# Optimization experiments

Hardware: AMD Instinct MI355X
Metric: run time of the kernel (lower is better)

Reference implementation:

```python
import jax, jax.numpy as jnp
import numpy as np

N, C, H, W = 8, 80, 200, 200
PRE_NMS_THRESH = 0.05
PRE_NMS_TOP_N = 1000
NMS_THRESH = 0.6
FPN_POST_NMS_TOP_N = 100
MIN_SIZE = 0.0
TO_REMOVE = 1.0
CLASS_OFFSET = 100000.0  # > any coordinate; separates classes for class-aware NMS


def setup_inputs() -> dict:
    key = jax.random.key(0)
    k1, k2, k3, k4, k5 = jax.random.split(key, 5)
    # logits shifted so sigmoid probs sit near the 0.05 threshold (realistic sparsity)
    box_cls = jax.random.normal(k1, (N, C, H, W), jnp.float32) - 3.0
    box_regression = jax.random.uniform(k2, (N, 4, H, W), jnp.float32) * 64.0
    centerness = jax.random.normal(k3, (N, 1, H, W), jnp.float32)
    locations = jax.random.uniform(k4, (H * W, 2), jnp.float32) * 1600.0
    image_sizes = jax.random.randint(k5, (N, 2), 800, 1600, jnp.int32)  # (h, w)
    return {"locations": locations, "box_cls": box_cls,
            "box_regression": box_regression, "centerness": centerness,
            "image_sizes": image_sizes}


def _pairwise_iou(boxes):
    x1, y1, x2, y2 = boxes[:, 0], boxes[:, 1], boxes[:, 2], boxes[:, 3]
    area = (x2 - x1 + TO_REMOVE) * (y2 - y1 + TO_REMOVE)  # [K]
    iw = jnp.clip(jnp.minimum(x2[:, None], x2[None, :]) - jnp.maximum(x1[:, None], x1[None, :]) + TO_REMOVE, 0.0)
    ih = jnp.clip(jnp.minimum(y2[:, None], y2[None, :]) - jnp.maximum(y1[:, None], y1[None, :]) + TO_REMOVE, 0.0)
    inter = iw * ih
    return inter / (area[:, None] + area[None, :] - inter)


def reference(locations, box_cls, box_regression, centerness, image_sizes):
    n, c, h, w = box_cls.shape
    # [N,C,H,W] -> [N,HW,C] probs; [N,4,H,W] -> [N,HW,4]; centerness -> [N,HW]
    cls_prob = jax.nn.sigmoid(box_cls.transpose(0, 2, 3, 1).reshape(n, -1, c))
    reg = box_regression.transpose(0, 2, 3, 1).reshape(n, -1, 4)
    cent = jax.nn.sigmoid(centerness.transpose(0, 2, 3, 1).reshape(n, -1))

    def per_image(p, r, ct, hw):
        # candidate mask on raw class probs (before centerness weighting), as in source
        cand = p > PRE_NMS_THRESH                      # [HW, C]
        scores = p * ct[:, None]                       # [HW, C]
        flat = jnp.where(cand, scores, -jnp.inf).reshape(-1)
        top_s, top_i = jax.lax.top_k(flat, PRE_NMS_TOP_N)   # sorted desc
        loc_idx = top_i // c
        labels = top_i % c + 1
        valid = top_s > 0.0
        l2 = locations[loc_idx]                        # [K, 2]
        rr = r[loc_idx]                                # [K, 4]
        boxes = jnp.concatenate([l2 - rr[:, :2], l2 + rr[:, 2:]], axis=-1)
        ih = hw[0].astype(jnp.float32)
        iw = hw[1].astype(jnp.float32)
        boxes = jnp.stack([jnp.clip(boxes[:, 0], 0.0, iw - 1.0),
                           jnp.clip(boxes[:, 1], 0.0, ih - 1.0),
                           jnp.clip(boxes[:, 2], 0.0, iw - 1.0),
                           jnp.clip(boxes[:, 3], 0.0, ih - 1.0)], axis=-1)
        bw = boxes[:, 2] - boxes[:, 0] + TO_REMOVE
        bh = boxes[:, 3] - boxes[:, 1] + TO_REMOVE
        valid = valid & (bw >= MIN_SIZE) & (bh >= MIN_SIZE)
        # class-aware NMS via per-class coordinate offset
        ob = boxes + labels.astype(jnp.float32)[:, None] * CLASS_OFFSET
        iou = _pairwise_iou(ob)                        # [K, K]
        K = PRE_NMS_TOP_N
        idxs = jnp.arange(K)
        def body(supp, i):
            keep_i = valid[i] & jnp.logical_not(supp[i])
            supp = supp | (keep_i & (iou[i] > NMS_THRESH) & (idxs != i))
            return supp, keep_i
        _, keep = jax.lax.scan(body, jnp.zeros(K, dtype=bool), idxs)
        fscores = jnp.where(keep & valid, top_s, -jnp.inf)
        fs, fi = jax.lax.top_k(fscores, FPN_POST_NMS_TOP_N)
        fv = fs > 0.0
        fb = boxes[fi] * fv[:, None].astype(boxes.dtype)
        fl = jnp.where(fv, labels[fi], 0).astype(jnp.float32)
        out_s = jnp.where(fv, jnp.sqrt(jnp.where(fv, fs, 1.0)), 0.0)  # sqrt of cls*centerness
        # [K_post, 6] = x1,y1,x2,y2,score,label
        return jnp.concatenate([fb, out_s[:, None], fl[:, None]], axis=-1)

    return jax.vmap(per_image)(cls_prob, reg, cent, image_sizes)
```

## Files before the change

### kernel.cpp

```cpp
#include <hip/hip_runtime.h>
#include <math.h>

#define NIMG 8
#define NCLS 80
#define HW 40000
#define M (NCLS*HW)
#define UBINS 4096
#define CANDL 4096
#define SPILL_CAP 65536
#define BCAP 1024
#define TOPK 1000
#define OUTK 100
#define PRE_T 0.05f
#define NMS_T 0.6f
#define FLOOR_BITS 0x3E800000u
#define FLOOR_SAFE 0.2494f

__device__ unsigned int       g_scnt[NIMG][32];
__device__ unsigned int       g_ovf[NIMG];
__device__ float              g_xthr[NIMG * HW];
__device__ float              g_sct[NIMG * HW];
__device__ unsigned long long g_key[NIMG][SPILL_CAP];

__device__ __forceinline__ float sigmoid_exact(float x){
    return 1.0f / (1.0f + expf(-x));
}

__device__ __forceinline__ unsigned long long shfl_xor_u64(unsigned long long v, int j){
    int lo = __shfl_xor((int)(unsigned int)(v & 0xffffffffull), j);
    int hi = __shfl_xor((int)(unsigned int)(v >> 32), j);
    return ((unsigned long long)(unsigned int)hi << 32) | (unsigned long long)(unsigned int)lo;
}

__global__ void k0_init(const float* __restrict__ cent){
    int t = blockIdx.x * blockDim.x + threadIdx.x;
    if (t < NIMG * 32) ((unsigned int*)g_scnt)[t] = 0u;
    if (t < NIMG) g_ovf[t] = 0u;
    if (t < NIMG * HW){
        float pct = sigmoid_exact(cent[t]);
        g_sct[t] = pct;
        float a = FLOOR_SAFE / pct;
        float xt;
        if (a >= 1.0f) xt = 3.0e38f;
        else {
            float am = fminf(a, 0.98f);
            xt = logf(am / (1.0f - am));
        }
        g_xthr[t] = xt;
    }
}

__global__ void __launch_bounds__(1024) k1_spill(const float* __restrict__ cls){
    const int n   = blockIdx.y;
    const int tid = threadIdx.x;
    const int e0  = blockIdx.x * 4096 + tid * 4;
    __shared__ unsigned long long skey[BCAP];
    __shared__ unsigned int lcnt, lbase;
    if (tid == 0) lcnt = 0u;
    __syncthreads();
    if (e0 < M){
        const int c  = e0 / HW;
        const int hw = e0 - c * HW;
        float4 x  = *(const float4*)(cls + (size_t)n * M + e0);
        float4 th = *(const float4*)(g_xthr + n * HW + hw);
        #define SPILL1(J, XV) \
        if (XV >= (J==0?th.x:J==1?th.y:J==2?th.z:th.w)){ \
            float p_ = sigmoid_exact(XV); \
            if (p_ > PRE_T){ \
                float s_ = p_ * g_sct[n * HW + hw + J]; \
                unsigned long long key_ = ((unsigned long long)__float_as_uint(s_) << 32) \
                    | (unsigned long long)(0xFFFFFFFFu - (unsigned int)((hw + J) * NCLS + c)); \
                unsigned int pp_ = atomicAdd(&lcnt, 1u); \
                if (pp_ < BCAP) skey[pp_] = key_; \
            } \
        }
        SPILL1(0, x.x)
        SPILL1(1, x.y)
        SPILL1(2, x.z)
        SPILL1(3, x.w)
        #undef SPILL1
    }
    __syncthreads();
    unsigned int raw = lcnt;
    unsigned int cnt = raw < BCAP ? raw : BCAP;
    if (tid == 0){
        lbase = cnt ? atomicAdd(&g_scnt[n][0], cnt) : 0u;
        if (raw > BCAP) g_ovf[n] = 1u;
    }
    __syncthreads();
    unsigned int base = lbase;
    for (unsigned int i = tid; i < cnt; i += 1024){
        unsigned int pos = base + i;
        if (pos < SPILL_CAP) g_key[n][pos] = skey[i];
    }
}

struct SelPhase {
    unsigned int hist[UBINS];
    unsigned int cs[256];
    unsigned int wtot[4];
    unsigned long long keysL[CANDL];
};
struct NmsPhase {
    float ox1[TOPK], oy1[TOPK], ox2[TOPK], oy2[TOPK], oar[TOPK];
    float bxs[TOPK][4];
    float sc[TOPK];
    int   lab[TOPK];
    int   keeplist[OUTK];
    unsigned int  Wc[16][80];
    unsigned int  ctot[80];
    unsigned int  coff[81];
    unsigned int  wcnt[16];
    unsigned short ord[1024];
    unsigned char validf[TOPK];
    unsigned char supp[TOPK];
    unsigned char keepf[1024];
};
union KU { SelPhase sel; NmsPhase nms; };

#define REGSTEP(K_, J_) { \
    unsigned long long pa = shfl_xor_u64(va, (J_)); \
    unsigned long long pb = shfl_xor_u64(vb, (J_)); \
    bool fa = ((tid & (J_)) == 0); \
    bool da = ((tid & (K_)) == 0); \
    bool db = (((tid + 1024) & (K_)) == 0); \
    va = (fa == da) ? (va > pa ? va : pa) : (va < pa ? va : pa); \
    vb = (fa == db) ? (vb > pb ? vb : pb) : (vb < pb ? vb : pb); \
}

__global__ void __launch_bounds__(1024) k2_select_nms(const float* __restrict__ cls,
                                                      const float* __restrict__ loc,
                                                      const float* __restrict__ reg,
                                                      const int*   __restrict__ imsz,
                                                      float* __restrict__ out){
    const int n = blockIdx.x;
    const int tid = threadIdx.x;
    const int lane = tid & 63;
    const int wv   = tid >> 6;
    __shared__ KU u;
    __shared__ unsigned long long stop[TOPK];
    __shared__ unsigned int lcnt, s_cut, s_flag, s_nmsfb, s_cnt, s_c, s_csn, s_Cest, s_srtbad;

    for (int i = tid; i < UBINS; i += 1024) u.sel.hist[i] = 0u;
    if (tid == 0){ s_nmsfb = 0u; s_srtbad = 0u; s_c = 0xFFFFFFFFu; s_csn = 0u;
                   s_Cest = 0u; s_cut = 0u; lcnt = 0u; }
    if (tid < TOPK) stop[tid] = 0ull;
    __syncthreads();

    unsigned int scnt_raw = g_scnt[n][0];
    unsigned int ovf_f    = g_ovf[n];
    unsigned int S = scnt_raw < SPILL_CAP ? scnt_raw : SPILL_CAP;

    for (unsigned int i = tid; i < S; i += 1024){
        unsigned long long k = g_key[n][i];
        float s = __uint_as_float((unsigned int)(k >> 32));
        atomicAdd(&u.sel.hist[(int)(s * 4096.0f)], 1u);
    }
    __syncthreads();
    if (tid < 256){
        unsigned int s = 0;
        int base = tid * 16;
        #pragma unroll
        for (int i = 0; i < 16; ++i) s += u.sel.hist[base + i];
        u.sel.cs[tid] = s;
    }
    __syncthreads();
    if (tid < 256){
        unsigned int v = u.sel.cs[tid];
        #pragma unroll
        for (int d = 1; d < 64; d <<= 1){
            unsigned int t = __shfl_down(v, d);
            if (lane + d < 64) v += t;
        }
        if (lane == 0) u.sel.wtot[wv] = v;
        u.sel.cs[tid] = v;
    }
    __syncthreads();
    if (tid < 256){
        unsigned int tail = 0;
        for (int w = wv + 1; w < 4; ++w) tail += u.sel.wtot[w];
        u.sel.cs[tid] += tail;
    }
    __syncthreads();
    if (tid < 256){
        unsigned int a = u.sel.cs[tid];
        unsigned int b = (tid == 255) ? 0u : u.sel.cs[tid + 1];
        if (a >= TOPK && b < TOPK){ s_c = (unsigned int)tid; s_csn = b; }
    }
    __syncthreads();
    if (wv == 0 && s_c != 0xFFFFFFFFu){
        unsigned int cst = s_c;
        unsigned int h = (lane < 16) ? u.sel.hist[cst * 16 + lane] : 0u;
        #pragma unroll
        for (int d = 1; d < 16; d <<= 1){
            unsigned int t = __shfl_down(h, d);
            if (lane + d < 16) h += t;
        }
        unsigned int gs  = h + s_csn;
        unsigned int gsn = __shfl_down(gs, 1);
        if (lane == 15) gsn = s_csn;
        if (lane < 16 && gs >= TOPK && gsn < TOPK){ s_cut = cst * 16 + lane; s_Cest = gs; }
    }
    __syncthreads();
    if (tid == 0){
        unsigned int c025 = u.sel.cs[64];
        s_flag = (scnt_raw > SPILL_CAP) || ovf_f || (s_c == 0xFFFFFFFFu) ||
                 (c025 < TOPK) || (s_Cest > CANDL) ? 1u : 0u;
    }
    __syncthreads();

    if (s_flag){
        for (int i = tid; i < UBINS; i += 1024) u.sel.hist[i] = 0u;
        __syncthreads();
        const float* cls_n = cls + (size_t)n * M;
        const float* sct_n = g_sct + n * HW;
        for (int e = tid; e < M; e += 1024){
            float p = sigmoid_exact(cls_n[e]);
            if (p > PRE_T){
                int c = e / HW; int hw = e - c * HW;
                float s = p * sct_n[hw];
                atomicAdd(&u.sel.hist[(int)(s * 4096.0f)], 1u);
            }
        }
        __syncthreads();
        if (tid < 256){
            unsigned int s = 0;
            int base = tid * 16;
            #pragma unroll
            for (int i = 0; i < 16; ++i) s += u.sel.hist[base + i];
            u.sel.cs[tid] = s;
        }
        __syncthreads();
        if (tid == 0){
            unsigned int acc = 0; int cut = 0; int c = 255;
            for (; c >= 0; --c){ if (acc + u.sel.cs[c] >= TOPK) break; acc += u.sel.cs[c]; }
            if (c >= 0){
                int b = c*16 + 15;
                for (;; --b){ acc += u.sel.hist[b]; if (acc >= TOPK || b == c*16) break; }
                cut = b;
            }
            while (acc > CANDL && cut < UBINS){ acc -= u.sel.hist[cut]; cut++; }
            s_cut = (unsigned int)cut;
        }
        __syncthreads();
        unsigned int cutb = s_cut;
        for (int e = tid; e < M; e += 1024){
            float p = sigmoid_exact(cls_n[e]);
            if (p > PRE_T){
                int c = e / HW; int hw = e - c * HW;
                float s = p * sct_n[hw];
                if ((int)(s * 4096.0f) >= (int)cutb){
                    unsigned int pos = atomicAdd(&lcnt, 1u);
                    if (pos < CANDL){
                        unsigned int idx = (unsigned int)(hw * NCLS + c);
                        u.sel.keysL[pos] = ((unsigned long long)__float_as_uint(s) << 32)
                                         | (unsigned long long)(0xFFFFFFFFu - idx);
                    }
                }
            }
        }
    } else {
        unsigned int cutb = s_cut;
        for (unsigned int i = tid; i < S; i += 1024){
            unsigned long long k = g_key[n][i];
            float s = __uint_as_float((unsigned int)(k >> 32));
            bool pass = ((unsigned int)(int)(s * 4096.0f)) >= cutb;
            unsigned long long mb = __ballot(pass);
            unsigned int wcnt_ = (unsigned int)__popcll(mb);
            unsigned int base = 0;
            if (lane == 0 && wcnt_) base = atomicAdd(&lcnt, wcnt_);
            base = (unsigned int)__builtin_amdgcn_readfirstlane((int)base);
            if (pass){
                unsigned int p = base + (unsigned int)__popcll(mb & ((1ull << lane) - 1ull));
                if (p < CANDL) u.sel.keysL[p] = k;
            }
        }
    }
    __syncthreads();

    int C = (int)(lcnt < CANDL ? lcnt : CANDL);
    unsigned long long kk = 0ull;
    if (C <= 2048){
        for (int i = C + tid; i < 2048; i += 1024) u.sel.keysL[i] = 0ull;
        __syncthreads();
        unsigned long long va = u.sel.keysL[tid];
        unsigned long long vb = u.sel.keysL[tid + 1024];
        REGSTEP(2,1)
        REGSTEP(4,2)  REGSTEP(4,1)
        REGSTEP(8,4)  REGSTEP(8,2)  REGSTEP(8,1)
        REGSTEP(16,8) REGSTEP(16,4) REGSTEP(16,2) REGSTEP(16,1)
        REGSTEP(32,16) REGSTEP(32,8) REGSTEP(32,4) REGSTEP(32,2) REGSTEP(32,1)
        REGSTEP(64,32) REGSTEP(64,16) REGSTEP(64,8) REGSTEP(64,4) REGSTEP(64,2) REGSTEP(64,1)
        for (int k = 128; k <= 2048; k <<= 1){
            if (k == 2048){
                unsigned long long mx = va > vb ? va : vb;
                unsigned long long mn = va > vb ? vb : va;
                va = mx; vb = mn;
            }
            u.sel.keysL[tid] = va; u.sel.keysL[tid + 1024] = vb;
            __syncthreads();
            for (int j = (k == 2048) ? 512 : (k >> 1); j >= 64; j >>= 1){
                int i  = ((tid & ~(j - 1)) << 1) | (tid & (j - 1));
                int p2 = i | j;
                unsigned long long a = u.sel.keysL[i];
                unsigned long long b = u.sel.keysL[p2];
                bool up = ((i & k) == 0);
                if (up ? (a < b) : (a > b)){ u.sel.keysL[i] = b; u.sel.keysL[p2] = a; }
                __syncthreads();
            }
            va = u.sel.keysL[tid]; vb = u.sel.keysL[tid + 1024];
            REGSTEP(k,32) REGSTEP(k,16) REGSTEP(k,8) REGSTEP(k,4) REGSTEP(k,2) REGSTEP(k,1)
        }
        u.sel.keysL[tid] = va; u.sel.keysL[tid + 1024] = vb;
        __syncthreads();
        bool bad = (u.sel.keysL[tid] < u.sel.keysL[tid + 1]);
        if (tid <= 1022) bad = bad || (u.sel.keysL[tid + 1024] < u.sel.keysL[tid + 1025]);
        if (bad) atomicOr(&s_srtbad, 1u);
        __syncthreads();
        if (s_srtbad){
            if (tid == 0) lcnt = 0u;
            __syncthreads();
            unsigned int cutb = s_cut;
            if (s_flag){
                const float* cls_n = cls + (size_t)n * M;
                const float* sct_n = g_sct + n * HW;
                for (int e = tid; e < M; e += 1024){
                    float p = sigmoid_exact(cls_n[e]);
                    if (p > PRE_T){
                        int c = e / HW; int hw = e - c * HW;
                        float s = p * sct_n[hw];
                        if ((int)(s * 4096.0f) >= (int)cutb){
                            unsigned int pos = atomicAdd(&lcnt, 1u);
                            if (pos < CANDL){
                                unsigned int idx = (unsigned int)(hw * NCLS + c);
                                u.sel.keysL[pos] = ((unsigned long long)__float_as_uint(s) << 32)
                                                 | (unsigned long long)(0xFFFFFFFFu - idx);
                            }
                        }
                    }
                }
            } else {
                for (unsigned int i = tid; i < S; i += 1024){
                    unsigned long long k = g_key[n][i];
                    float s = __uint_as_float((unsigned int)(k >> 32));
                    bool pass = ((unsigned int)(int)(s * 4096.0f)) >= cutb;
                    unsigned long long mb = __ballot(pass);
                    unsigned int wcnt_ = (unsigned int)__popcll(mb);
                    unsigned int base = 0;
                    if (lane == 0 && wcnt_) base = atomicAdd(&lcnt, wcnt_);
                    base = (unsigned int)__builtin_amdgcn_readfirstlane((int)base);
                    if (pass){
                        unsigned int p = base + (unsigned int)__popcll(mb & ((1ull << lane) - 1ull));
                        if (p < CANDL) u.sel.keysL[p] = k;
                    }
                }
            }
            __syncthreads();
            int C2 = (int)(lcnt < CANDL ? lcnt : CANDL);
            for (int i = C2 + tid; i < 2048; i += 1024) u.sel.keysL[i] = 0ull;
            __syncthreads();
            for (int k = 2; k <= 2048; k <<= 1){
                for (int j = k >> 1; j > 0; j >>= 1){
                    int i  = ((tid & ~(j - 1)) << 1) | (tid & (j - 1));
                    int p2 = i | j;
                    unsigned long long a = u.sel.keysL[i];
                    unsigned long long b = u.sel.keysL[p2];
                    bool up = ((i & k) == 0);
                    if (up ? (a < b) : (a > b)){ u.sel.keysL[i] = b; u.sel.keysL[p2] = a; }
                    __syncthreads();
                }
            }
        }
        kk = (tid < TOPK) ? u.sel.keysL[tid] : 0ull;
    } else {
        for (int i = tid; i < C; i += 1024){
            unsigned long long k = u.sel.keysL[i];
            int rank = 0;
            for (int j = 0; j < C; ++j) rank += (u.sel.keysL[j] > k) ? 1 : 0;
            if (rank < TOPK) stop[rank] = k;
        }
        __syncthreads();
        kk = (tid < TOPK) ? stop[tid] : 0ull;
    }
    __syncthreads();

    float rx1 = 0.f, ry1 = 0.f, rx2 = -1.f, ry2 = -1.f, rar = 1.f;
    float ihh = (float)imsz[2*n + 0];
    float iww = (float)imsz[2*n + 1];

    u.nms.keepf[tid] = 0;
    { unsigned int* wz = &u.nms.Wc[0][0];
      for (int i = tid; i < 16*80; i += 1024) wz[i] = 0u; }

    if (tid < TOPK){
        unsigned int bits = (unsigned int)(kk >> 32);
        float s = __uint_as_float(bits);
        u.nms.supp[tid] = 0;
        if (s > 0.0f){
            unsigned int idx = 0xFFFFFFFFu - (unsigned int)(kk & 0xFFFFFFFFull);
            int hw = (int)(idx / NCLS);
            int c  = (int)(idx % NCLS);
            int l  = c + 1;
            float x  = loc[2*hw], y = loc[2*hw + 1];
            float r0 = reg[((size_t)n*4 + 0)*HW + hw];
            float r1 = reg[((size_t)n*4 + 1)*HW + hw];
            float r2 = reg[((size_t)n*4 + 2)*HW + hw];
            float r3 = reg[((size_t)n*4 + 3)*HW + hw];
            float x1 = fminf(fmaxf(x - r0, 0.0f), iww - 1.0f);
            float y1 = fminf(fmaxf(y - r1, 0.0f), ihh - 1.0f);
            float x2 = fminf(fmaxf(x + r2, 0.0f), iww - 1.0f);
            float y2 = fminf(fmaxf(y + r3, 0.0f), ihh - 1.0f);
            u.nms.bxs[tid][0] = x1; u.nms.bxs[tid][1] = y1;
            u.nms.bxs[tid][2] = x2; u.nms.bxs[tid][3] = y2;
            float off = (float)l * 100000.0f;
            float a1 = x1 + off, b1 = y1 + off, a2 = x2 + off, b2 = y2 + off;
            float ar = (a2 - a1 + 1.0f) * (b2 - b1 + 1.0f);
            u.nms.ox1[tid] = a1; u.nms.oy1[tid] = b1;
            u.nms.ox2[tid] = a2; u.nms.oy2[tid] = b2; u.nms.oar[tid] = ar;
            rx1 = a1; ry1 = b1; rx2 = a2; ry2 = b2; rar = ar;
            u.nms.sc[tid] = s; u.nms.lab[tid] = l; u.nms.validf[tid] = 1;
        } else {
            u.nms.validf[tid] = 0; u.nms.sc[tid] = 0.0f; u.nms.lab[tid] = 0;
            u.nms.bxs[tid][0] = u.nms.bxs[tid][1] = 0.0f;
            u.nms.bxs[tid][2] = u.nms.bxs[tid][3] = 0.0f;
            u.nms.ox1[tid] = 0.f; u.nms.oy1[tid] = 0.f;
            u.nms.ox2[tid] = -1.f; u.nms.oy2[tid] = -1.f; u.nms.oar[tid] = 1.f;
        }
    }
    __syncthreads();

    int mk = -1;
    if (tid < TOPK && u.nms.validf[tid]) mk = u.nms.lab[tid] - 1;
    if (mk >= 0) atomicAdd(&u.nms.Wc[wv][mk], 1u);
    __syncthreads();
    if (tid < NCLS){
        unsigned int acc = 0;
        for (int w = 0; w < 16; ++w){
            unsigned int v = u.nms.Wc[w][tid];
            u.nms.Wc[w][tid] = acc;
            acc += v;
        }
        u.nms.ctot[tid] = acc;
        if (acc > 64) atomicOr(&s_nmsfb, 1u);
    }
    __syncthreads();
    if (wv == 0){
        unsigned int v = u.nms.ctot[lane];
        unsigned int inc = v;
        #pragma unroll
        for (int d = 1; d < 64; d <<= 1){
            unsigned int t = __shfl_up(inc, d);
            if (lane >= d) inc += t;
        }
        u.nms.coff[lane + 1] = inc;
        if (lane == 0) u.nms.coff[0] = 0u;
        unsigned int base = __shfl(inc, 63);
        unsigned int inc2 = (lane < 16) ? u.nms.ctot[64 + lane] : 0u;
        #pragma unroll
        for (int d = 1; d < 16; d <<= 1){
            unsigned int t = __shfl_up(inc2, d);
            if (lane >= d) inc2 += t;
        }
        if (lane < 16) u.nms.coff[65 + lane] = base + inc2;
    }
    __syncthreads();

    if (!s_nmsfb){
        int below = 0;
        for (int l = 0; l < 64; ++l){
            int ok = __shfl(mk, l);
            below += (l < lane && ok == mk) ? 1 : 0;
        }
        if (mk >= 0){
            unsigned int pos = u.nms.coff[mk] + u.nms.Wc[wv][mk] + (unsigned int)below;
            u.nms.ord[pos] = (unsigned short)tid;
        }
        __syncthreads();

        for (int k = wv; k < NCLS; k += 16){
            int base = (int)u.nms.coff[k];
            int ck   = (int)u.nms.coff[k + 1] - base;
            if (ck <= 0) continue;
            int rr = (lane < ck) ? (int)u.nms.ord[base + lane] : -1;
            float bx1 = 0.f, by1 = 0.f, bx2 = -1.f, by2 = -1.f, bar = 1.f;
            if (rr >= 0){
                bx1 = u.nms.ox1[rr]; by1 = u.nms.oy1[rr];
                bx2 = u.nms.ox2[rr]; by2 = u.nms.oy2[rr]; bar = u.nms.oar[rr];
            }
            int sup = 0;
            for (int p = 0; p < ck; ++p){
                int keep_p = !__shfl(sup, p);
                if (keep_p){
                    float px1 = __shfl(bx1, p), py1 = __shfl(by1, p);
                    float px2 = __shfl(bx2, p), py2 = __shfl(by2, p);
                    float par = __shfl(bar, p);
                    if (lane > p && rr >= 0){
                        float ix1 = fmaxf(px1, bx1);
                        float iy1 = fmaxf(py1, by1);
                        float ix2 = fminf(px2, bx2);
                        float iy2 = fminf(py2, by2);
                        float iw_ = fmaxf(ix2 - ix1 + 1.0f, 0.0f);
                        float ih_ = fmaxf(iy2 - iy1 + 1.0f, 0.0f);
                        float inter = iw_ * ih_;
                        float iou = inter / (par + bar - inter);
                        if (iou > NMS_T) sup = 1;
                    }
                }
            }
            if (rr >= 0) u.nms.keepf[rr] = sup ? 0 : 1;
        }
        __syncthreads();

        int kf = (int)u.nms.keepf[tid];
        unsigned long long mb = __ballot(kf != 0);
        if (lane == 0) u.nms.wcnt[wv] = (unsigned int)__popcll(mb);
        __syncthreads();
        if (wv == 0){
            unsigned int v = (lane < 16) ? u.nms.wcnt[lane] : 0u;
            unsigned int orig = v;
            for (int d = 1; d < 16; d <<= 1){
                unsigned int t = __shfl_up(v, d);
                if (lane >= d) v += t;
            }
            if (lane < 16) u.nms.wcnt[lane] = v - orig;
            if (lane == 15) s_cnt = (v < OUTK ? v : OUTK);
        }
        __syncthreads();
        if (kf){
            unsigned int slot = u.nms.wcnt[wv] + (unsigned int)__popcll(mb & ((1ull << lane) - 1ull));
            if (slot < OUTK) u.nms.keeplist[slot] = tid;
        }
    } else {
        int cnt = 0;
        for (int i = 0; i < TOPK; ++i){
            bool keep_i = u.nms.validf[i] && !u.nms.supp[i];
            if (keep_i){
                if (tid == 0) u.nms.keeplist[cnt] = i;
                if (tid < TOPK && tid != i){
                    float ix1 = fmaxf(u.nms.ox1[i], rx1);
                    float iy1 = fmaxf(u.nms.oy1[i], ry1);
                    float ix2 = fminf(u.nms.ox2[i], rx2);
                    float iy2 = fminf(u.nms.oy2[i], ry2);
                    float iw_ = fmaxf(ix2 - ix1 + 1.0f, 0.0f);
                    float ih_ = fmaxf(iy2 - iy1 + 1.0f, 0.0f);
                    float inter = iw_ * ih_;
                    float iou = inter / (u.nms.oar[i] + rar - inter);
                    if (iou > NMS_T) u.nms.supp[tid] = 1;
                }
                cnt++;
                __syncthreads();
                if (cnt == OUTK) break;
            }
        }
        if (tid == 0) s_cnt = (unsigned int)(cnt < OUTK ? cnt : OUTK);
    }
    __syncthreads();

    int cnt = (int)s_cnt;
    if (tid < OUTK){
        float r0=0.f,r1=0.f,r2=0.f,r3=0.f,r4=0.f,r5=0.f;
        if (tid < cnt){
            int i = u.nms.keeplist[tid];
            r0 = u.nms.bxs[i][0]; r1 = u.nms.bxs[i][1];
            r2 = u.nms.bxs[i][2]; r3 = u.nms.bxs[i][3];
            r4 = sqrtf(u.nms.sc[i]); r5 = (float)u.nms.lab[i];
        }
        float* o = out + ((size_t)n*OUTK + tid)*6;
        o[0]=r0; o[1]=r1; o[2]=r2; o[3]=r3; o[4]=r4; o[5]=r5;
    }
}

extern "C" void kernel_launch(void* const* d_in, const int* in_sizes, int n_in,
                              void* d_out, int out_size, void* d_ws, size_t ws_size,
                              hipStream_t stream){
    const float* loc  = (const float*)d_in[0];
    const float* cls  = (const float*)d_in[1];
    const float* reg  = (const float*)d_in[2];
    const float* cent = (const float*)d_in[3];
    const int*   imsz = (const int*)d_in[4];
    float* out = (float*)d_out;

    hipLaunchKernelGGL(k0_init,       dim3(625),                 dim3(512),  0, stream, cent);
    hipLaunchKernelGGL(k1_spill,      dim3((M+4095)/4096, NIMG), dim3(1024), 0, stream, cls);
    hipLaunchKernelGGL(k2_select_nms, dim3(NIMG),                dim3(1024), 0, stream,
                       cls, loc, reg, imsz, out);
}
```

Measured before the change: 257.0 us.

## Build score histogram in spill kernel and add 1024-wide register bitonic sort

```diff
diff --git a/kernel.cpp b/kernel.cpp
--- a/kernel.cpp
+++ b/kernel.cpp
@@ -18,6 +18,7 @@
 
 __device__ unsigned int       g_scnt[NIMG][32];
 __device__ unsigned int       g_ovf[NIMG];
+__device__ unsigned int       g_hist[NIMG][UBINS];
 __device__ float              g_xthr[NIMG * HW];
 __device__ float              g_sct[NIMG * HW];
 __device__ unsigned long long g_key[NIMG][SPILL_CAP];
@@ -36,6 +37,7 @@
     int t = blockIdx.x * blockDim.x + threadIdx.x;
     if (t < NIMG * 32) ((unsigned int*)g_scnt)[t] = 0u;
     if (t < NIMG) g_ovf[t] = 0u;
+    if (t < NIMG * UBINS) ((unsigned int*)g_hist)[t] = 0u;
     if (t < NIMG * HW){
         float pct = sigmoid_exact(cent[t]);
         g_sct[t] = pct;
@@ -70,6 +72,7 @@
                 float s_ = p_ * g_sct[n * HW + hw + J]; \
                 unsigned long long key_ = ((unsigned long long)__float_as_uint(s_) << 32) \
                     | (unsigned long long)(0xFFFFFFFFu - (unsigned int)((hw + J) * NCLS + c)); \
+                atomicAdd(&g_hist[n][(int)(s_ * 4096.0f)], 1u); \
                 unsigned int pp_ = atomicAdd(&lcnt, 1u); \
                 if (pp_ < BCAP) skey[pp_] = key_; \
             } \
@@ -127,6 +130,12 @@
     va = (fa == da) ? (va > pa ? va : pa) : (va < pa ? va : pa); \
     vb = (fa == db) ? (vb > pb ? vb : pb) : (vb < pb ? vb : pb); \
 }
+#define REGSTEP1(K_, J_) { \
+    unsigned long long pa = shfl_xor_u64(va, (J_)); \
+    bool fa = ((tid & (J_)) == 0); \
+    bool da = ((tid & (K_)) == 0); \
+    va = (fa == da) ? (va > pa ? va : pa) : (va < pa ? va : pa); \
+}
 
 __global__ void __launch_bounds__(1024) k2_select_nms(const float* __restrict__ cls,
                                                       const float* __restrict__ loc,
@@ -141,7 +150,7 @@
     __shared__ unsigned long long stop[TOPK];
     __shared__ unsigned int lcnt, s_cut, s_flag, s_nmsfb, s_cnt, s_c, s_csn, s_Cest, s_srtbad;
 
-    for (int i = tid; i < UBINS; i += 1024) u.sel.hist[i] = 0u;
+    for (int i = tid; i < UBINS; i += 1024) u.sel.hist[i] = g_hist[n][i];
     if (tid == 0){ s_nmsfb = 0u; s_srtbad = 0u; s_c = 0xFFFFFFFFu; s_csn = 0u;
                    s_Cest = 0u; s_cut = 0u; lcnt = 0u; }
     if (tid < TOPK) stop[tid] = 0ull;
@@ -151,12 +160,6 @@
     unsigned int ovf_f    = g_ovf[n];
     unsigned int S = scnt_raw < SPILL_CAP ? scnt_raw : SPILL_CAP;
 
-    for (unsigned int i = tid; i < S; i += 1024){
-        unsigned long long k = g_key[n][i];
-        float s = __uint_as_float((unsigned int)(k >> 32));
-        atomicAdd(&u.sel.hist[(int)(s * 4096.0f)], 1u);
-    }
-    __syncthreads();
     if (tid < 256){
         unsigned int s = 0;
         int base = tid * 16;
@@ -280,7 +283,38 @@
 
     int C = (int)(lcnt < CANDL ? lcnt : CANDL);
     unsigned long long kk = 0ull;
-    if (C <= 2048){
+    if (C <= 1024){
+        for (int i = C + tid; i < 1024; i += 1024) u.sel.keysL[i] = 0ull;
+        __syncthreads();
+        unsigned long long va = u.sel.keysL[tid];
+        REGSTEP1(2,1)
+        REGSTEP1(4,2)  REGSTEP1(4,1)
+        REGSTEP1(8,4)  REGSTEP1(8,2)  REGSTEP1(8,1)
+        REGSTEP1(16,8) REGSTEP1(16,4) REGSTEP1(16,2) REGSTEP1(16,1)
+        REGSTEP1(32,16) REGSTEP1(32,8) REGSTEP1(32,4) REGSTEP1(32,2) REGSTEP1(32,1)
+        REGSTEP1(64,32) REGSTEP1(64,16) REGSTEP1(64,8) REGSTEP1(64,4) REGSTEP1(64,2) REGSTEP1(64,1)
+        for (int k = 128; k <= 1024; k <<= 1){
+            u.sel.keysL[tid] = va;
+            __syncthreads();
+            for (int j = k >> 1; j >= 64; j >>= 1){
+                if (tid < 512){
+                    int i  = ((tid & ~(j - 1)) << 1) | (tid & (j - 1));
+                    int p2 = i | j;
+                    unsigned long long a = u.sel.keysL[i];
+                    unsigned long long b = u.sel.keysL[p2];
+                    bool up = ((i & k) == 0);
+                    if (up ? (a < b) : (a > b)){ u.sel.keysL[i] = b; u.sel.keysL[p2] = a; }
+                }
+                __syncthreads();
+            }
+            va = u.sel.keysL[tid];
+            REGSTEP1(k,32) REGSTEP1(k,16) REGSTEP1(k,8) REGSTEP1(k,4) REGSTEP1(k,2) REGSTEP1(k,1)
+        }
+        u.sel.keysL[tid] = va;
+        __syncthreads();
+        if (tid <= 1022 && u.sel.keysL[tid] < u.sel.keysL[tid + 1]) atomicOr(&s_srtbad, 1u);
+        __syncthreads();
+    } else if (C <= 2048){
         for (int i = C + tid; i < 2048; i += 1024) u.sel.keysL[i] = 0ull;
         __syncthreads();
         unsigned long long va = u.sel.keysL[tid];
@@ -317,61 +351,6 @@
         if (tid <= 1022) bad = bad || (u.sel.keysL[tid + 1024] < u.sel.keysL[tid + 1025]);
         if (bad) atomicOr(&s_srtbad, 1u);
         __syncthreads();
-        if (s_srtbad){
-            if (tid == 0) lcnt = 0u;
-            __syncthreads();
-            unsigned int cutb = s_cut;
-            if (s_flag){
-                const float* cls_n = cls + (size_t)n * M;
-                const float* sct_n = g_sct + n * HW;
-                for (int e = tid; e < M; e += 1024){
-                    float p = sigmoid_exact(cls_n[e]);
-                    if (p > PRE_T){
-                        int c = e / HW; int hw = e - c * HW;
-                        float s = p * sct_n[hw];
-                        if ((int)(s * 4096.0f) >= (int)cutb){
-                            unsigned int pos = atomicAdd(&lcnt, 1u);
-                            if (pos < CANDL){
-                                unsigned int idx = (unsigned int)(hw * NCLS + c);
-                                u.sel.keysL[pos] = ((unsigned long long)__float_as_uint(s) << 32)
-                                                 | (unsigned long long)(0xFFFFFFFFu - idx);
-                            }
-                        }
-                    }
-                }
-            } else {
-                for (unsigned int i = tid; i < S; i += 1024){
-                    unsigned long long k = g_key[n][i];
-                    float s = __uint_as_float((unsigned int)(k >> 32));
-                    bool pass = ((unsigned int)(int)(s * 4096.0f)) >= cutb;
-                    unsigned long long mb = __ballot(pass);
-                    unsigned int wcnt_ = (unsigned int)__popcll(mb);
-                    unsigned int base = 0;
-                    if (lane == 0 && wcnt_) base = atomicAdd(&lcnt, wcnt_);
-                    base = (unsigned int)__builtin_amdgcn_readfirstlane((int)base);
-                    if (pass){
-                        unsigned int p = base + (unsigned int)__popcll(mb & ((1ull << lane) - 1ull));
-                        if (p < CANDL) u.sel.keysL[p] = k;
-                    }
-                }
-            }
-            __syncthreads();
-            int C2 = (int)(lcnt < CANDL ? lcnt : CANDL);
-            for (int i = C2 + tid; i < 2048; i += 1024) u.sel.keysL[i] = 0ull;
-            __syncthreads();
-            for (int k = 2; k <= 2048; k <<= 1){
-                for (int j = k >> 1; j > 0; j >>= 1){
-                    int i  = ((tid & ~(j - 1)) << 1) | (tid & (j - 1));
-                    int p2 = i | j;
-                    unsigned long long a = u.sel.keysL[i];
-                    unsigned long long b = u.sel.keysL[p2];
-                    bool up = ((i & k) == 0);
-                    if (up ? (a < b) : (a > b)){ u.sel.keysL[i] = b; u.sel.keysL[p2] = a; }
-                    __syncthreads();
-                }
-            }
-        }
-        kk = (tid < TOPK) ? u.sel.keysL[tid] : 0ull;
     } else {
         for (int i = tid; i < C; i += 1024){
             unsigned long long k = u.sel.keysL[i];
@@ -380,8 +359,65 @@
             if (rank < TOPK) stop[rank] = k;
         }
         __syncthreads();
-        kk = (tid < TOPK) ? stop[tid] : 0ull;
-    }
+        if (tid < TOPK) u.sel.keysL[tid] = stop[tid];
+        __syncthreads();
+    }
+
+    if (s_srtbad){
+        if (tid == 0) lcnt = 0u;
+        __syncthreads();
+        unsigned int cutb = s_cut;
+        if (s_flag){
+            const float* cls_n = cls + (size_t)n * M;
+            const float* sct_n = g_sct + n * HW;
+            for (int e = tid; e < M; e += 1024){
+                float p = sigmoid_exact(cls_n[e]);
+                if (p > PRE_T){
+                    int c = e / HW; int hw = e - c * HW;
+                    float s = p * sct_n[hw];
+                    if ((int)(s * 4096.0f) >= (int)cutb){
+                        unsigned int pos = atomicAdd(&lcnt, 1u);
+                        if (pos < CANDL){
+                            unsigned int idx = (unsigned int)(hw * NCLS + c);
+                            u.sel.keysL[pos] = ((unsigned long long)__float_as_uint(s) << 32)
+                                             | (unsigned long long)(0xFFFFFFFFu - idx);
+                        }
+                    }
+                }
+            }
+        } else {
+            for (unsigned int i = tid; i < S; i += 1024){
+                unsigned long long k = g_key[n][i];
+                float s = __uint_as_float((unsigned int)(k >> 32));
+                bool pass = ((unsigned int)(int)(s * 4096.0f)) >= cutb;
+                unsigned long long mb = __ballot(pass);
+                unsigned int wcnt_ = (unsigned int)__popcll(mb);
+                unsigned int base = 0;
+                if (lane == 0 && wcnt_) base = atomicAdd(&lcnt, wcnt_);
+                base = (unsigned int)__builtin_amdgcn_readfirstlane((int)base);
+                if (pass){
+                    unsigned int p = base + (unsigned int)__popcll(mb & ((1ull << lane) - 1ull));
+                    if (p < CANDL) u.sel.keysL[p] = k;
+                }
+            }
+        }
+        __syncthreads();
+        int C2 = (int)(lcnt < CANDL ? lcnt : CANDL);
+        for (int i = C2 + tid; i < 2048; i += 1024) u.sel.keysL[i] = 0ull;
+        __syncthreads();
+        for (int k = 2; k <= 2048; k <<= 1){
+            for (int j = k >> 1; j > 0; j >>= 1){
+                int i  = ((tid & ~(j - 1)) << 1) | (tid & (j - 1));
+                int p2 = i | j;
+                unsigned long long a = u.sel.keysL[i];
+                unsigned long long b = u.sel.keysL[p2];
+                bool up = ((i & k) == 0);
+                if (up ? (a < b) : (a > b)){ u.sel.keysL[i] = b; u.sel.keysL[p2] = a; }
+                __syncthreads();
+            }
+        }
+    }
+    kk = (tid < TOPK) ? u.sel.keysL[tid] : 0ull;
     __syncthreads();
 
     float rx1 = 0.f, ry1 = 0.f, rx2 = -1.f, ry2 = -1.f, rar = 1.f;
```

Result: faster. 249.3 us (-3.0%).
